# Kernel tuning notes

Hardware: AMD Instinct MI355X
Metric: run time of the kernel (lower is better)

Reference implementation:

```python
import jax, jax.numpy as jnp
import numpy as np

D = 160          # volume side
WIN = 32         # spatial window size (box filter, matches fftconvolve with ones kernel)
NUM_MIN = 100    # minimum count constraint (constraint.min_number_from_ratio)
K_CCL = 16       # fixed number of 6-neighbor min-propagation sweeps (CCL definition)
NUM_BINS = 4096  # fixed histogram bins replacing data-dependent np.unique
VALUES = (0, 1, 2)
LIST_LABELS = (1,)
NUM_LABELS = 2
HALF = WIN // 2


def _box1d(x, w, ax):
    # 'same' box-sum along one axis via cumsum (== fftconvolve with ones(w))
    left = w // 2
    right = w - 1 - left
    x = jnp.moveaxis(x, ax, -1)
    pads = [(0, 0)] * (x.ndim - 1) + [(left, right)]
    c = jnp.cumsum(jnp.pad(x, pads), axis=-1)
    c = jnp.pad(c, [(0, 0)] * (x.ndim - 1) + [(1, 0)])
    out = c[..., w:] - c[..., :-w]
    return jnp.moveaxis(out, -1, ax)


def box_sum(x, w):
    for ax in range(x.ndim):
        x = _box1d(x, w, ax)
    return x


def _shift(a, s, ax, fill):
    # shift by s along ax, filling vacated border with `fill`
    r = jnp.roll(a, s, axis=ax)
    n = a.shape[ax]
    co = jnp.arange(n).reshape([n if i == ax else 1 for i in range(a.ndim)])
    bad = (co < s) if s > 0 else (co >= n + s)
    return jnp.where(bad, fill, r)


def label_size_map(seg):
    # create_label_size_map: connected-component labeling (6-connectivity,
    # K_CCL min-propagation sweeps) then replace each component by its size.
    n_vox = seg.size
    big = jnp.int32(n_vox + 2)
    idx = (jnp.arange(n_vox, dtype=jnp.int32) + 1).reshape(seg.shape)
    lab0 = jnp.where(seg, idx, big)

    def step(_, lab):
        m = lab
        for ax in range(seg.ndim):
            for s in (1, -1):
                m = jnp.minimum(m, _shift(lab, s, ax, big))
        return jnp.where(seg, m, big)

    lab = jax.lax.fori_loop(0, K_CCL, step, lab0)
    labels = jnp.where(seg, lab, 0)  # background -> label 0
    cnt = jnp.zeros(n_vox + 1, jnp.float32).at[labels.ravel()].add(1.0)
    return jnp.where(seg, cnt[labels], 0.0)


def _proba_weights(candidates, mean_list):
    # create_probability_weights: reciprocal-histogram weighting over rounded
    # mean component sizes (fixed NUM_BINS integer bins; bin 0 = non-candidate).
    pw = jnp.ones_like(candidates)
    for m in mean_list:
        possible = candidates * m
        idx = jnp.clip(jnp.round(possible), 0, NUM_BINS - 1).astype(jnp.int32)
        hist = jnp.zeros(NUM_BINS, jnp.float32).at[idx.ravel()].add(1.0)
        numb = jnp.sum(hist[1:])
        rec = jnp.where(hist[1:] > 0, numb / jnp.maximum(hist[1:], 1.0), 0.0)
        ph = rec / jnp.sum(rec)
        ph_full = jnp.concatenate([jnp.zeros(1, jnp.float32), ph])
        pw = pw * ph_full[idx]
    return pw / jnp.sum(pw)


def setup_inputs() -> dict:
    key = jax.random.key(0)
    data = jax.random.randint(key, (D, D, D), 0, 3).astype(jnp.float32)
    return {"data": data}


def reference(data):
    data = jnp.round(data)
    inner = tuple(s - 2 * HALF for s in data.shape)
    final = jnp.pad(jnp.ones(inner, jnp.float32), [(HALF, HALF)] * 3)
    mean_list = []
    valid_others = []
    for v in VALUES:
        seg = data == v
        segf = seg.astype(jnp.float32)
        lsize = label_size_map(seg)
        cw = box_sum(segf, WIN)                              # counts_window
        valid = (cw > max(NUM_MIN, 1)).astype(jnp.float32)   # valid_places
        cs = box_sum(lsize * valid, WIN)                     # counts_size
        mean = jnp.where(cw > 0, cs / jnp.maximum(cw, 1.0), 0.0)
        if v in LIST_LABELS:
            mean_list.append(mean)
            final = final * valid
        else:
            valid_others.append(valid)
    for vo in valid_others:
        final = final + vo
    num_labels_add = max(NUM_LABELS - len(LIST_LABELS), 0)
    candidates = (final >= num_labels_add + 1).astype(jnp.float32)
    proba_fin = _proba_weights(candidates, mean_list)
    return candidates, proba_fin
```

## Files before the change

kernel.cpp:

```cpp
#include <hip/hip_runtime.h>
#include <cmath>

#define D 160
#define DD (D*D)
#define NVOX (D*D*D)
#define BIGV (NVOX + 2)
#define NBINS 4096
#define HALF 16
#define RGRID 800
#define SGRID 1000
#define ZGRID 1000
#define CGRID 800

template<int MODE>
__device__ __forceinline__ void rot_block(
    const void* __restrict__ vin, unsigned* __restrict__ out, int bi, int tid)
{
    __shared__ unsigned tin[32][161];
    __shared__ unsigned filt[160][33];
    int L0 = bi * 32;
    size_t base = (size_t)L0 * D;

    if (MODE == 0) {
        const float4* s4 = (const float4*)((const float*)vin + base);
        for (int i = tid; i < 32 * (D / 4); i += 512) {
            float4 v = s4[i];
            int e = i * 4, r = e / D, c = e - r * D;
            float rr;
            rr = rintf(v.x); tin[r][c]   = (rr==0.f) | ((rr==1.f)?0x10000u:0u);
            rr = rintf(v.y); tin[r][c+1] = (rr==0.f) | ((rr==1.f)?0x10000u:0u);
            rr = rintf(v.z); tin[r][c+2] = (rr==0.f) | ((rr==1.f)?0x10000u:0u);
            rr = rintf(v.w); tin[r][c+3] = (rr==0.f) | ((rr==1.f)?0x10000u:0u);
        }
    } else {
        const uint4* s4 = (const uint4*)((const unsigned*)vin + base);
        for (int i = tid; i < 32 * (D / 4); i += 512) {
            uint4 v = s4[i];
            int e = i * 4, r = e / D, c = e - r * D;
            tin[r][c] = v.x; tin[r][c+1] = v.y; tin[r][c+2] = v.z; tin[r][c+3] = v.w;
        }
    }
    __syncthreads();

    {
        int r = tid & 31, s = tid >> 5;
        int i0 = 10 * s;
        const unsigned* ln = tin[r];
        unsigned sum = 0u;
        int jlo = i0 - 16; if (jlo < 0) jlo = 0;
        int jhi = i0 + 15; if (jhi > D - 1) jhi = D - 1;
        for (int j = jlo; j <= jhi; ++j) sum += ln[j];
        #pragma unroll
        for (int k = 0; k < 10; ++k) {
            int i = i0 + k;
            filt[i][r] = sum;
            int add = i + 16, rem = i - 16;
            if (add <= D - 1) sum += ln[add];
            if (rem >= 0)     sum -= ln[rem];
        }
    }
    __syncthreads();

    int r = tid & 31;
    for (int c = (tid >> 5); c < D; c += 16)
        out[(size_t)c * DD + L0 + r] = filt[c][r];
}

__global__ __launch_bounds__(256) void box_rot_f32_g_kernel(
    const int* __restrict__ lab, const int* __restrict__ cnt,
    const unsigned* __restrict__ cwp, float* __restrict__ out)
{
    __shared__ float tin[32][161];
    __shared__ float filt[160][33];
    int L0 = blockIdx.x * 32;
    size_t base = (size_t)L0 * D;

    const int4*  lab4 = (const int4*)(lab + base);
    const uint4* cw4  = (const uint4*)(cwp + base);
    for (int i = threadIdx.x; i < 32 * (D / 4); i += 256) {
        int4 l = lab4[i];
        uint4 cw = cw4[i];
        int e = i * 4, r = e / D, c = e - r * D;
        tin[r][c]   = (l.x != BIGV && (cw.x >> 16) > 100u) ? (float)cnt[l.x] : 0.f;
        tin[r][c+1] = (l.y != BIGV && (cw.y >> 16) > 100u) ? (float)cnt[l.y] : 0.f;
        tin[r][c+2] = (l.z != BIGV && (cw.z >> 16) > 100u) ? (float)cnt[l.z] : 0.f;
        tin[r][c+3] = (l.w != BIGV && (cw.w >> 16) > 100u) ? (float)cnt[l.w] : 0.f;
    }
    __syncthreads();

    {
        int r = threadIdx.x & 31, s = threadIdx.x >> 5;
        int i0 = 20 * s;
        const float* ln = tin[r];
        float sum = 0.f;
        int jlo = i0 - 16; if (jlo < 0) jlo = 0;
        int jhi = i0 + 15; if (jhi > D - 1) jhi = D - 1;
        for (int j = jlo; j <= jhi; ++j) sum += ln[j];
        #pragma unroll 4
        for (int k = 0; k < 20; ++k) {
            int i = i0 + k;
            filt[i][r] = sum;
            int add = i + 16, rem = i - 16;
            if (add <= D - 1) sum += ln[add];
            if (rem >= 0)     sum -= ln[rem];
        }
    }
    __syncthreads();

    int r = threadIdx.x & 31;
    for (int c = (threadIdx.x >> 5); c < D; c += 8)
        out[(size_t)c * DD + L0 + r] = filt[c][r];
}

__global__ __launch_bounds__(256) void box_rot_f32_kernel(
    const float* __restrict__ fin, float* __restrict__ out)
{
    __shared__ float tin[32][161];
    __shared__ float filt[160][33];
    int L0 = blockIdx.x * 32;
    size_t base = (size_t)L0 * D;

    const float4* s4 = (const float4*)(fin + base);
    for (int i = threadIdx.x; i < 32 * (D / 4); i += 256) {
        float4 v = s4[i];
        int e = i * 4, r = e / D, c = e - r * D;
        tin[r][c] = v.x; tin[r][c+1] = v.y; tin[r][c+2] = v.z; tin[r][c+3] = v.w;
    }
    __syncthreads();

    {
        int r = threadIdx.x & 31, s = threadIdx.x >> 5;
        int i0 = 20 * s;
        const float* ln = tin[r];
        float sum = 0.f;
        int jlo = i0 - 16; if (jlo < 0) jlo = 0;
        int jhi = i0 + 15; if (jhi > D - 1) jhi = D - 1;
        for (int j = jlo; j <= jhi; ++j) sum += ln[j];
        #pragma unroll 4
        for (int k = 0; k < 20; ++k) {
            int i = i0 + k;
            filt[i][r] = sum;
            int add = i + 16, rem = i - 16;
            if (add <= D - 1) sum += ln[add];
            if (rem >= 0)     sum -= ln[rem];
        }
    }
    __syncthreads();

    int r = threadIdx.x & 31;
    for (int c = (threadIdx.x >> 5); c < D; c += 8)
        out[(size_t)c * DD + L0 + r] = filt[c][r];
}

__global__ __launch_bounds__(256) void box_rot_fin_kernel(
    const float* __restrict__ fin, const unsigned* __restrict__ cwp,
    unsigned short* __restrict__ idxbuf, int* __restrict__ partial)
{
    __shared__ float tin[32][161];
    __shared__ float filt[160][33];
    __shared__ int lh[NBINS];
    for (int i = threadIdx.x; i < NBINS; i += 256) lh[i] = 0;

    int L0 = blockIdx.x * 32;
    size_t base = (size_t)L0 * D;
    const float4* s4 = (const float4*)(fin + base);
    for (int i = threadIdx.x; i < 32 * (D / 4); i += 256) {
        float4 v = s4[i];
        int e = i * 4, r = e / D, c = e - r * D;
        tin[r][c] = v.x; tin[r][c+1] = v.y; tin[r][c+2] = v.z; tin[r][c+3] = v.w;
    }
    __syncthreads();

    {
        int r = threadIdx.x & 31, s = threadIdx.x >> 5;
        int i0 = 20 * s;
        const float* ln = tin[r];
        float sum = 0.f;
        int jlo = i0 - 16; if (jlo < 0) jlo = 0;
        int jhi = i0 + 15; if (jhi > D - 1) jhi = D - 1;
        for (int j = jlo; j <= jhi; ++j) sum += ln[j];
        #pragma unroll 4
        for (int k = 0; k < 20; ++k) {
            int i = i0 + k;
            filt[i][r] = sum;
            int add = i + 16, rem = i - 16;
            if (add <= D - 1) sum += ln[add];
            if (rem >= 0)     sum -= ln[rem];
        }
    }
    __syncthreads();

    int r = threadIdx.x & 31;
    int L = L0 + r;
    int y = L / D, z = L - (L / D) * D;
    bool byz = (y >= HALF && y < D - HALF && z >= HALF && z < D - HALF);
    int wy = min(y + 15, D - 1) - max(y - 16, 0) + 1;
    int wz = min(z + 15, D - 1) - max(z - 16, 0) + 1;
    for (int c = (threadIdx.x >> 5); c < D; c += 8) {
        int p = c * DD + L;
        unsigned pk = cwp[p];
        unsigned cw0 = pk & 0xFFFFu;
        unsigned cw1 = pk >> 16;
        int wx = min(c + 15, D - 1) - max(c - 16, 0) + 1;
        unsigned cw2 = (unsigned)(wx * wy * wz) - cw0 - cw1;
        float v0 = (cw0 > 100u) ? 1.f : 0.f;
        float v1 = (cw1 > 100u) ? 1.f : 0.f;
        float v2 = (cw2 > 100u) ? 1.f : 0.f;
        float border = (byz && c >= HALF && c < D - HALF) ? 1.f : 0.f;
        float cd = (border * v1 + v0 + v2 >= 2.f) ? 1.f : 0.f;
        float mean = (cw1 > 0u) ? filt[c][r] / fmaxf((float)cw1, 1.f) : 0.f;
        int idx = (int)rintf(cd * mean);
        idx = min(max(idx, 0), NBINS - 1);
        idxbuf[p] = (unsigned short)idx;
        if (idx != 0) atomicAdd(&lh[idx], 1);
    }
    __syncthreads();
    int* po = partial + blockIdx.x * NBINS;
    for (int i = threadIdx.x; i < NBINS; i += 256) po[i] = lh[i];
}

__device__ __forceinline__ int min6(int c, int a, int b, int d, int e, int f, int g) {
    if (c == BIGV) return BIGV;
    return min(min(min(c, a), min(b, d)), min(min(e, f), g));
}

__device__ __forceinline__ int4 min7_run(int4 c, int lm, int rm,
                                         int4 ym, int4 yp, int4 xm, int4 xp) {
    int4 o;
    o.x = min6(c.x, lm,  c.y, ym.x, yp.x, xm.x, xp.x);
    o.y = min6(c.y, c.x, c.z, ym.y, yp.y, xm.y, xp.y);
    o.z = min6(c.z, c.y, c.w, ym.z, yp.z, xm.z, xp.z);
    o.w = min6(c.w, c.z, rm,  ym.w, yp.w, xm.w, xp.w);
    return o;
}

__device__ __forceinline__ void wave_count(int l, int lane, int* __restrict__ cnt) {
    unsigned long long remaining = __ballot(l != BIGV);
    while (remaining) {
        int leader = __ffsll((unsigned long long)remaining) - 1;
        int ll = __shfl(l, leader, 64);
        unsigned long long mm = __ballot(l == ll);
        if (lane == leader) atomicAdd(&cnt[ll], (int)__popcll(mm & remaining));
        remaining &= ~mm;
    }
}

__device__ __forceinline__ int4 cls4(float4 v, int p0) {
    int4 l;
    l.x = (rintf(v.x) == 1.f) ? (p0 + 1) : BIGV;
    l.y = (rintf(v.y) == 1.f) ? (p0 + 2) : BIGV;
    l.z = (rintf(v.z) == 1.f) ? (p0 + 3) : BIGV;
    l.w = (rintf(v.w) == 1.f) ? (p0 + 4) : BIGV;
    return l;
}

struct LabLd {
    const int* __restrict__ a;
    __device__ __forceinline__ int4 v(int p) const { return ((const int4*)a)[p >> 2]; }
    __device__ __forceinline__ int  s(int p) const { return a[p]; }
};
struct DataLd {
    const float* __restrict__ a;
    __device__ __forceinline__ int4 v(int p) const { return cls4(((const float4*)a)[p >> 2], p); }
    __device__ __forceinline__ int  s(int p) const { return (rintf(a[p]) == 1.f) ? (p + 1) : BIGV; }
};

template<typename LDT, int COUNT>
__device__ __forceinline__ void sweep_block(
    LDT ld, int* __restrict__ outp, int* __restrict__ cnt, int b, int tid)
{
    const int4 BIG4 = make_int4(BIGV, BIGV, BIGV, BIGV);
    int sb = (b & 7) * (SGRID / 8) + (b >> 3);
    int lane = tid & 63;
    int wv   = tid >> 6;
    int wbase = sb * 4096 + wv * 512;
    int pA = wbase + 4 * lane;
    int pB = pA + 256;

    int4 cA = ld.v(pA), cB = ld.v(pB);

    int zA = pA % D, zB = pB % D;
    int lmA = __shfl_up(cA.w, 1);
    int rmA = __shfl_down(cA.x, 1);
    int lmB = __shfl_up(cB.w, 1);
    int rmB = __shfl_down(cB.x, 1);
    int stA = __shfl(cB.x, 0, 64);
    int stB = __shfl(cA.w, 63, 64);
    if (lane == 63) rmA = stA;
    if (lane == 0)  lmB = stB;
    if (zA == 0)          lmA = BIGV;
    else if (lane == 0)   lmA = ld.s(pA - 1);
    if (zA == D - 4)      rmA = BIGV;
    if (zB == 0)          lmB = BIGV;
    if (zB == D - 4)      rmB = BIGV;
    else if (lane == 63)  rmB = ld.s(pB + 4);

    int rA = pA / D, yA = rA % D, xA = rA / D;
    int4 ylA = (yA > 0)     ? ld.v(pA - D)  : BIG4;
    int4 yhA = (yA < D - 1) ? ld.v(pA + D)  : BIG4;
    int4 xlA = (xA > 0)     ? ld.v(pA - DD) : BIG4;
    int4 xhA = (xA < D - 1) ? ld.v(pA + DD) : BIG4;
    int4 oA = min7_run(cA, lmA, rmA, ylA, yhA, xlA, xhA);

    int rB = pB / D, yB = rB % D, xB = rB / D;
    int4 ylB = (yB > 0)     ? ld.v(pB - D)  : BIG4;
    int4 yhB = (yB < D - 1) ? ld.v(pB + D)  : BIG4;
    int4 xlB = (xB > 0)     ? ld.v(pB - DD) : BIG4;
    int4 xhB = (xB < D - 1) ? ld.v(pB + DD) : BIG4;
    int4 oB = min7_run(cB, lmB, rmB, ylB, yhB, xlB, xhB);

    int4* out4 = (int4*)outp;
    out4[pA >> 2] = oA; out4[pB >> 2] = oB;

    if (COUNT) {
        wave_count(oA.x, lane, cnt);
        wave_count(oA.y, lane, cnt);
        wave_count(oA.z, lane, cnt);
        wave_count(oA.w, lane, cnt);
        wave_count(oB.x, lane, cnt);
        wave_count(oB.y, lane, cnt);
        wave_count(oB.z, lane, cnt);
        wave_count(oB.w, lane, cnt);
    }
}

__global__ __launch_bounds__(512) void ccl_sweep_kernel(
    const int* __restrict__ lab, int* __restrict__ outp)
{
    LabLd ld{lab};
    sweep_block<LabLd, 0>(ld, outp, nullptr, blockIdx.x, threadIdx.x);
}

__global__ __launch_bounds__(512) void ccl_sweep_count_kernel(
    const int* __restrict__ lab, int* __restrict__ outp, int* __restrict__ cnt)
{
    LabLd ld{lab};
    sweep_block<LabLd, 1>(ld, outp, cnt, blockIdx.x, threadIdx.x);
}

template<int MODE>
__global__ __launch_bounds__(512) void sweep_rot_kernel(
    const float* __restrict__ data, const int* __restrict__ labsrc,
    int* __restrict__ swdst,
    const void* __restrict__ rin, unsigned* __restrict__ rout)
{
    if ((int)blockIdx.x < SGRID) {
        if (MODE == 0) {
            DataLd ld{data};
            sweep_block<DataLd, 0>(ld, swdst, nullptr, blockIdx.x, threadIdx.x);
        } else {
            LabLd ld{labsrc};
            sweep_block<LabLd, 0>(ld, swdst, nullptr, blockIdx.x, threadIdx.x);
        }
    } else {
        rot_block<MODE>(rin, rout, blockIdx.x - SGRID, threadIdx.x);
    }
}

__global__ __launch_bounds__(512) void sweep_zero_kernel(
    const int* __restrict__ labsrc, int* __restrict__ swdst,
    int* __restrict__ zbuf, int* __restrict__ ticket)
{
    if ((int)blockIdx.x < SGRID) {
        LabLd ld{labsrc};
        sweep_block<LabLd, 0>(ld, swdst, nullptr, blockIdx.x, threadIdx.x);
    } else {
        int zb = blockIdx.x - SGRID;
        int t = (zb * 512 + threadIdx.x) * 2;
        const int4 z4 = make_int4(0, 0, 0, 0);
        ((int4*)zbuf)[t] = z4; ((int4*)zbuf)[t + 1] = z4;
        if (zb == 0 && threadIdx.x == 0) { zbuf[NVOX] = 0; ticket[0] = 0; }
    }
}

__global__ __launch_bounds__(512) void sweep_cand_kernel(
    const int* __restrict__ labsrc, int* __restrict__ swdst,
    const unsigned* __restrict__ cwp, float* __restrict__ cand)
{
    if ((int)blockIdx.x < SGRID) {
        LabLd ld{labsrc};
        sweep_block<LabLd, 0>(ld, swdst, nullptr, blockIdx.x, threadIdx.x);
        return;
    }
    int t0 = (blockIdx.x - SGRID) * 512 + threadIdx.x;
    const uint4* cw4 = (const uint4*)cwp;
    float4* c4 = (float4*)cand;
    for (int q = t0; q < NVOX / 4; q += CGRID * 512) {
        int p0 = q * 4;
        int z0 = p0 % D;
        int r  = p0 / D;
        int y  = r % D;
        int x  = r / D;
        int wy = min(y + 15, D - 1) - max(y - 16, 0) + 1;
        int wx = min(x + 15, D - 1) - max(x - 16, 0) + 1;
        bool bxy = (y >= HALF && y < D - HALF && x >= HALF && x < D - HALF);
        uint4 pk = cw4[q];
        float4 o;
        {
            unsigned c0 = pk.x & 0xFFFFu, c1 = pk.x >> 16;
            int z = z0, wz = min(z + 15, D - 1) - max(z - 16, 0) + 1;
            unsigned c2 = (unsigned)(wx * wy * wz) - c0 - c1;
            float v0 = (c0 > 100u) ? 1.f : 0.f, v1 = (c1 > 100u) ? 1.f : 0.f, v2 = (c2 > 100u) ? 1.f : 0.f;
            float border = (bxy && z >= HALF && z < D - HALF) ? 1.f : 0.f;
            o.x = (border * v1 + v0 + v2 >= 2.f) ? 1.f : 0.f;
        }
        {
            unsigned c0 = pk.y & 0xFFFFu, c1 = pk.y >> 16;
            int z = z0 + 1, wz = min(z + 15, D - 1) - max(z - 16, 0) + 1;
            unsigned c2 = (unsigned)(wx * wy * wz) - c0 - c1;
            float v0 = (c0 > 100u) ? 1.f : 0.f, v1 = (c1 > 100u) ? 1.f : 0.f, v2 = (c2 > 100u) ? 1.f : 0.f;
            float border = (bxy && z >= HALF && z < D - HALF) ? 1.f : 0.f;
            o.y = (border * v1 + v0 + v2 >= 2.f) ? 1.f : 0.f;
        }
        {
            unsigned c0 = pk.z & 0xFFFFu, c1 = pk.z >> 16;
            int z = z0 + 2, wz = min(z + 15, D - 1) - max(z - 16, 0) + 1;
            unsigned c2 = (unsigned)(wx * wy * wz) - c0 - c1;
            float v0 = (c0 > 100u) ? 1.f : 0.f, v1 = (c1 > 100u) ? 1.f : 0.f, v2 = (c2 > 100u) ? 1.f : 0.f;
            float border = (bxy && z >= HALF && z < D - HALF) ? 1.f : 0.f;
            o.z = (border * v1 + v0 + v2 >= 2.f) ? 1.f : 0.f;
        }
        {
            unsigned c0 = pk.w & 0xFFFFu, c1 = pk.w >> 16;
            int z = z0 + 3, wz = min(z + 15, D - 1) - max(z - 16, 0) + 1;
            unsigned c2 = (unsigned)(wx * wy * wz) - c0 - c1;
            float v0 = (c0 > 100u) ? 1.f : 0.f, v1 = (c1 > 100u) ? 1.f : 0.f, v2 = (c2 > 100u) ? 1.f : 0.f;
            float border = (bxy && z >= HALF && z < D - HALF) ? 1.f : 0.f;
            o.w = (border * v1 + v0 + v2 >= 2.f) ? 1.f : 0.f;
        }
        c4[q] = o;
    }
}

__global__ __launch_bounds__(256) void hist_rp_kernel(
    const int* __restrict__ partial, int* __restrict__ hist,
    float* __restrict__ ph_full, float* __restrict__ Sout,
    int* __restrict__ ticket)
{
    int t = threadIdx.x;
    int bin = blockIdx.x * 256 + t;
    int s = 0;
    #pragma unroll 4
    for (int b = 0; b < RGRID; ++b) s += partial[b * NBINS + bin];
    __hip_atomic_store(&hist[bin], s, __ATOMIC_RELAXED, __HIP_MEMORY_SCOPE_AGENT);
    __threadfence();
    __syncthreads();
    __shared__ int lastblk;
    if (t == 0) lastblk = (atomicAdd(ticket, 1) == gridDim.x - 1) ? 1 : 0;
    __syncthreads();
    if (!lastblk) return;

    __shared__ float red[256];
    int hv[16];
    #pragma unroll
    for (int k = 0; k < 16; ++k)
        hv[k] = __hip_atomic_load(&hist[t + k * 256], __ATOMIC_RELAXED,
                                  __HIP_MEMORY_SCOPE_AGENT);

    float loc = 0.f;
    #pragma unroll
    for (int k = 0; k < 16; ++k) {
        int b = t + k * 256;
        if (b >= 1) loc += (float)hv[k];
    }
    red[t] = loc; __syncthreads();
    for (int o = 128; o > 0; o >>= 1) { if (t < o) red[t] += red[t + o]; __syncthreads(); }
    float numb = red[0]; __syncthreads();

    float rv[16];
    loc = 0.f;
    #pragma unroll
    for (int k = 0; k < 16; ++k) {
        int b = t + k * 256;
        float r = 0.f;
        if (b >= 1) {
            int h = hv[k];
            if (h > 0) r = numb / (float)h;
        }
        rv[k] = r;
        loc += r;
    }
    red[t] = loc; __syncthreads();
    for (int o = 128; o > 0; o >>= 1) { if (t < o) red[t] += red[t + o]; __syncthreads(); }
    float sumrec = red[0]; __syncthreads();
    float inv_sumrec = (sumrec > 0.f) ? 1.f / sumrec : 0.f;

    loc = 0.f;
    #pragma unroll
    for (int k = 0; k < 16; ++k) {
        int b = t + k * 256;
        float ph = (b >= 1) ? rv[k] * inv_sumrec : 0.f;
        ph_full[b] = ph;
        loc += ph * (float)hv[k];
    }
    red[t] = loc; __syncthreads();
    for (int o = 128; o > 0; o >>= 1) { if (t < o) red[t] += red[t + o]; __syncthreads(); }
    if (t == 0) Sout[0] = (red[0] > 0.f) ? red[0] : 1.f;
}

__global__ __launch_bounds__(256) void proba_kernel(
    const unsigned short* __restrict__ idxbuf,
    const float* __restrict__ ph_full, const float* __restrict__ Sv,
    float* __restrict__ outp)
{
    int t = blockIdx.x * blockDim.x + threadIdx.x;
    ushort4 i4 = ((const ushort4*)idxbuf)[t];
    float inv = 1.f / Sv[0];
    float4 o;
    o.x = ph_full[i4.x] * inv;
    o.y = ph_full[i4.y] * inv;
    o.z = ph_full[i4.z] * inv;
    o.w = ph_full[i4.w] * inv;
    ((float4*)outp)[t] = o;
}

extern "C" void kernel_launch(void* const* d_in, const int* in_sizes, int n_in,
                              void* d_out, int out_size, void* d_ws, size_t ws_size,
                              hipStream_t stream)
{
    const float* data = (const float*)d_in[0];
    float* out   = (float*)d_out;
    float* cand  = out;
    float* proba = out + NVOX;

    char* ws = (char*)d_ws;
    const size_t NB = (size_t)NVOX * sizeof(float);
    float* W1 = (float*)(ws);
    float* W2 = (float*)(ws + NB);
    float* W3 = (float*)(ws + 2 * NB);
    int*   W4 = (int*)(ws + 3 * NB);
    int*   cnt  = W4;
    float* ph   = (float*)(ws + 4 * NB + 16);
    int*   hist = (int*)  (ws + 4 * NB + 16 + NBINS * 4);
    float* Sv   = (float*)(ws + 4 * NB + 16 + 2 * NBINS * 4);
    int*   ticket = (int*)(ws + 4 * NB + 16 + 2 * NBINS * 4 + 8);
    unsigned short* idxbuf = (unsigned short*)cnt;
    int* partial = (int*)W2;

    dim3 rb(256), rg(RGRID);
    dim3 sbk(512);
    dim3 sg(SGRID);
    dim3 srg(SGRID + RGRID);
    dim3 szg(SGRID + ZGRID);
    dim3 scg(SGRID + CGRID);
    dim3 pb(256), pg(NVOX / 4 / 256);

    sweep_rot_kernel<0><<<srg, sbk, 0, stream>>>(data, nullptr, (int*)W2,
                                                 data, (unsigned*)W1);
    sweep_rot_kernel<1><<<srg, sbk, 0, stream>>>(nullptr, (int*)W2, W4,
                                                 W1, (unsigned*)W3);
    sweep_rot_kernel<1><<<srg, sbk, 0, stream>>>(nullptr, W4, (int*)W2,
                                                 W3, (unsigned*)W1);
    unsigned* cwp = (unsigned*)W1;

    sweep_zero_kernel<<<szg, sbk, 0, stream>>>((int*)W2, (int*)W3, W4, ticket);

    sweep_cand_kernel<<<scg, sbk, 0, stream>>>((int*)W3, (int*)W2, cwp, cand);

    for (int i = 0; i < 10; ++i) {
        const int* src = (i & 1) ? (int*)W3 : (int*)W2;
        int*       dst = (i & 1) ? (int*)W2 : (int*)W3;
        ccl_sweep_kernel<<<sg, sbk, 0, stream>>>(src, dst);
    }
    ccl_sweep_count_kernel<<<sg, sbk, 0, stream>>>((int*)W2, (int*)W3, cnt);
    int* lab = (int*)W3;

    box_rot_f32_g_kernel<<<rg, rb, 0, stream>>>(lab, cnt, cwp, W2);
    box_rot_f32_kernel<<<rg, rb, 0, stream>>>(W2, W3);
    box_rot_fin_kernel<<<rg, rb, 0, stream>>>(W3, cwp, idxbuf, partial);

    hist_rp_kernel<<<dim3(16), dim3(256), 0, stream>>>(partial, hist, ph, Sv, ticket);
    proba_kernel<<<pg, pb, 0, stream>>>(idxbuf, ph, Sv, proba);
}
```

Baseline: 386.8 us.

## Fuse z and y box-sum passes into one per-plane kernel using 2D prefix sums

Replaces the three rotating box-filter kernels with two. The first kernel loads a whole x-plane into shared memory, prefix-sums along z and slides a window along y. The second applies the x-window directly in the finalize/histogram kernel, which removes one full-volume write/read pass and one launch. The plane kernel runs only 160 blocks with 160 active threads each, and its serial prefix loop gives little parallelism. That may lower occupancy compared with the previous 800-block grid.

```diff
diff --git a/kernel.cpp b/kernel.cpp
--- a/kernel.cpp
+++ b/kernel.cpp
@@ -8,6 +8,7 @@
 #define NBINS 4096
 #define HALF 16
 #define RGRID 800
+#define FGRID 800
 #define SGRID 1000
 #define ZGRID 1000
 #define CGRID 800
@@ -66,153 +67,109 @@
         out[(size_t)c * DD + L0 + r] = filt[c][r];
 }
 
-__global__ __launch_bounds__(256) void box_rot_f32_g_kernel(
+__global__ __launch_bounds__(256) void plane_zy_g_kernel(
     const int* __restrict__ lab, const int* __restrict__ cnt,
     const unsigned* __restrict__ cwp, float* __restrict__ out)
 {
-    __shared__ float tin[32][161];
-    __shared__ float filt[160][33];
-    int L0 = blockIdx.x * 32;
-    size_t base = (size_t)L0 * D;
-
+    __shared__ float tin[160][161];
+    int x = blockIdx.x;
+    size_t base = (size_t)x * DD;
     const int4*  lab4 = (const int4*)(lab + base);
     const uint4* cw4  = (const uint4*)(cwp + base);
-    for (int i = threadIdx.x; i < 32 * (D / 4); i += 256) {
+    for (int i = threadIdx.x; i < DD / 4; i += 256) {
         int4 l = lab4[i];
         uint4 cw = cw4[i];
-        int e = i * 4, r = e / D, c = e - r * D;
-        tin[r][c]   = (l.x != BIGV && (cw.x >> 16) > 100u) ? (float)cnt[l.x] : 0.f;
-        tin[r][c+1] = (l.y != BIGV && (cw.y >> 16) > 100u) ? (float)cnt[l.y] : 0.f;
-        tin[r][c+2] = (l.z != BIGV && (cw.z >> 16) > 100u) ? (float)cnt[l.z] : 0.f;
-        tin[r][c+3] = (l.w != BIGV && (cw.w >> 16) > 100u) ? (float)cnt[l.w] : 0.f;
-    }
-    __syncthreads();
-
-    {
-        int r = threadIdx.x & 31, s = threadIdx.x >> 5;
-        int i0 = 20 * s;
-        const float* ln = tin[r];
-        float sum = 0.f;
-        int jlo = i0 - 16; if (jlo < 0) jlo = 0;
-        int jhi = i0 + 15; if (jhi > D - 1) jhi = D - 1;
-        for (int j = jlo; j <= jhi; ++j) sum += ln[j];
-        #pragma unroll 4
-        for (int k = 0; k < 20; ++k) {
-            int i = i0 + k;
-            filt[i][r] = sum;
-            int add = i + 16, rem = i - 16;
-            if (add <= D - 1) sum += ln[add];
-            if (rem >= 0)     sum -= ln[rem];
-        }
-    }
-    __syncthreads();
-
-    int r = threadIdx.x & 31;
-    for (int c = (threadIdx.x >> 5); c < D; c += 8)
-        out[(size_t)c * DD + L0 + r] = filt[c][r];
-}
-
-__global__ __launch_bounds__(256) void box_rot_f32_kernel(
-    const float* __restrict__ fin, float* __restrict__ out)
-{
-    __shared__ float tin[32][161];
-    __shared__ float filt[160][33];
-    int L0 = blockIdx.x * 32;
-    size_t base = (size_t)L0 * D;
-
-    const float4* s4 = (const float4*)(fin + base);
-    for (int i = threadIdx.x; i < 32 * (D / 4); i += 256) {
-        float4 v = s4[i];
-        int e = i * 4, r = e / D, c = e - r * D;
-        tin[r][c] = v.x; tin[r][c+1] = v.y; tin[r][c+2] = v.z; tin[r][c+3] = v.w;
-    }
-    __syncthreads();
-
-    {
-        int r = threadIdx.x & 31, s = threadIdx.x >> 5;
-        int i0 = 20 * s;
-        const float* ln = tin[r];
-        float sum = 0.f;
-        int jlo = i0 - 16; if (jlo < 0) jlo = 0;
-        int jhi = i0 + 15; if (jhi > D - 1) jhi = D - 1;
-        for (int j = jlo; j <= jhi; ++j) sum += ln[j];
-        #pragma unroll 4
-        for (int k = 0; k < 20; ++k) {
-            int i = i0 + k;
-            filt[i][r] = sum;
-            int add = i + 16, rem = i - 16;
-            if (add <= D - 1) sum += ln[add];
-            if (rem >= 0)     sum -= ln[rem];
-        }
-    }
-    __syncthreads();
-
-    int r = threadIdx.x & 31;
-    for (int c = (threadIdx.x >> 5); c < D; c += 8)
-        out[(size_t)c * DD + L0 + r] = filt[c][r];
-}
-
-__global__ __launch_bounds__(256) void box_rot_fin_kernel(
-    const float* __restrict__ fin, const unsigned* __restrict__ cwp,
+        int e = i * 4, y = e / D, z = e - y * D;
+        tin[y][z]   = (l.x != BIGV && (cw.x >> 16) > 100u) ? (float)cnt[l.x] : 0.f;
+        tin[y][z+1] = (l.y != BIGV && (cw.y >> 16) > 100u) ? (float)cnt[l.y] : 0.f;
+        tin[y][z+2] = (l.z != BIGV && (cw.z >> 16) > 100u) ? (float)cnt[l.z] : 0.f;
+        tin[y][z+3] = (l.w != BIGV && (cw.w >> 16) > 100u) ? (float)cnt[l.w] : 0.f;
+    }
+    __syncthreads();
+
+    if (threadIdx.x < D) {
+        float p = 0.f;
+        float* row = tin[threadIdx.x];
+        for (int z = 0; z < D; ++z) { p += row[z]; row[z] = p; }
+    }
+    __syncthreads();
+
+    if (threadIdx.x < D) {
+        int c = threadIdx.x;
+        int zhi = min(c + 15, D - 1);
+        bool hl = (c >= 16);
+        int zlo = c - 16;
+        float* op = out + base + c;
+        float S = 0.f;
+        for (int u = 0; u <= 15; ++u)
+            S += tin[u][zhi] - (hl ? tin[u][zlo] : 0.f);
+        for (int y = 0; y < D; ++y) {
+            op[(size_t)y * D] = S;
+            int add = y + 16, rem = y - 16;
+            if (add <= D - 1) S += tin[add][zhi] - (hl ? tin[add][zlo] : 0.f);
+            if (rem >= 0)     S -= tin[rem][zhi] - (hl ? tin[rem][zlo] : 0.f);
+        }
+    }
+}
+
+__global__ __launch_bounds__(256) void box_fin_x_kernel(
+    const float* __restrict__ zy, const unsigned* __restrict__ cwp,
     unsigned short* __restrict__ idxbuf, int* __restrict__ partial)
 {
-    __shared__ float tin[32][161];
-    __shared__ float filt[160][33];
+    __shared__ float tile[160][33];
     __shared__ int lh[NBINS];
     for (int i = threadIdx.x; i < NBINS; i += 256) lh[i] = 0;
 
-    int L0 = blockIdx.x * 32;
-    size_t base = (size_t)L0 * D;
-    const float4* s4 = (const float4*)(fin + base);
-    for (int i = threadIdx.x; i < 32 * (D / 4); i += 256) {
-        float4 v = s4[i];
-        int e = i * 4, r = e / D, c = e - r * D;
-        tin[r][c] = v.x; tin[r][c+1] = v.y; tin[r][c+2] = v.z; tin[r][c+3] = v.w;
-    }
-    __syncthreads();
-
-    {
-        int r = threadIdx.x & 31, s = threadIdx.x >> 5;
-        int i0 = 20 * s;
-        const float* ln = tin[r];
-        float sum = 0.f;
-        int jlo = i0 - 16; if (jlo < 0) jlo = 0;
-        int jhi = i0 + 15; if (jhi > D - 1) jhi = D - 1;
-        for (int j = jlo; j <= jhi; ++j) sum += ln[j];
-        #pragma unroll 4
-        for (int k = 0; k < 20; ++k) {
-            int i = i0 + k;
-            filt[i][r] = sum;
-            int add = i + 16, rem = i - 16;
-            if (add <= D - 1) sum += ln[add];
-            if (rem >= 0)     sum -= ln[rem];
-        }
+    int b = blockIdx.x;
+    int y  = b % D;
+    int zt = b / D;
+    int z0 = zt * 32;
+    int yb = y * D + z0;
+
+    for (int i = threadIdx.x; i < D * 8; i += 256) {
+        int x = i >> 3, q = i & 7;
+        float4 v = *(const float4*)(zy + (size_t)x * DD + yb + q * 4);
+        int c = q * 4;
+        tile[x][c] = v.x; tile[x][c+1] = v.y; tile[x][c+2] = v.z; tile[x][c+3] = v.w;
     }
     __syncthreads();
 
     int r = threadIdx.x & 31;
-    int L = L0 + r;
-    int y = L / D, z = L - (L / D) * D;
+    int s = threadIdx.x >> 5;
+    int z = z0 + r;
+    int i0 = 20 * s;
     bool byz = (y >= HALF && y < D - HALF && z >= HALF && z < D - HALF);
     int wy = min(y + 15, D - 1) - max(y - 16, 0) + 1;
     int wz = min(z + 15, D - 1) - max(z - 16, 0) + 1;
-    for (int c = (threadIdx.x >> 5); c < D; c += 8) {
-        int p = c * DD + L;
+
+    float S = 0.f;
+    int jlo = i0 - 16; if (jlo < 0) jlo = 0;
+    int jhi = i0 + 15; if (jhi > D - 1) jhi = D - 1;
+    for (int j = jlo; j <= jhi; ++j) S += tile[j][r];
+
+    #pragma unroll 4
+    for (int k = 0; k < 20; ++k) {
+        int i = i0 + k;
+        int p = i * DD + y * D + z;
         unsigned pk = cwp[p];
         unsigned cw0 = pk & 0xFFFFu;
         unsigned cw1 = pk >> 16;
-        int wx = min(c + 15, D - 1) - max(c - 16, 0) + 1;
+        int wx = min(i + 15, D - 1) - max(i - 16, 0) + 1;
         unsigned cw2 = (unsigned)(wx * wy * wz) - cw0 - cw1;
         float v0 = (cw0 > 100u) ? 1.f : 0.f;
         float v1 = (cw1 > 100u) ? 1.f : 0.f;
         float v2 = (cw2 > 100u) ? 1.f : 0.f;
-        float border = (byz && c >= HALF && c < D - HALF) ? 1.f : 0.f;
+        float border = (byz && i >= HALF && i < D - HALF) ? 1.f : 0.f;
         float cd = (border * v1 + v0 + v2 >= 2.f) ? 1.f : 0.f;
-        float mean = (cw1 > 0u) ? filt[c][r] / fmaxf((float)cw1, 1.f) : 0.f;
+        float mean = (cw1 > 0u) ? S / fmaxf((float)cw1, 1.f) : 0.f;
         int idx = (int)rintf(cd * mean);
         idx = min(max(idx, 0), NBINS - 1);
         idxbuf[p] = (unsigned short)idx;
         if (idx != 0) atomicAdd(&lh[idx], 1);
+
+        int add = i + 16, rem = i - 16;
+        if (add <= D - 1) S += tile[add][r];
+        if (rem >= 0)     S -= tile[rem][r];
     }
     __syncthreads();
     int* po = partial + blockIdx.x * NBINS;
@@ -359,7 +316,7 @@
 
 __global__ __launch_bounds__(512) void sweep_zero_kernel(
     const int* __restrict__ labsrc, int* __restrict__ swdst,
-    int* __restrict__ zbuf, int* __restrict__ ticket)
+    int* __restrict__ zbuf, int* __restrict__ tickets)
 {
     if ((int)blockIdx.x < SGRID) {
         LabLd ld{labsrc};
@@ -369,7 +326,9 @@
         int t = (zb * 512 + threadIdx.x) * 2;
         const int4 z4 = make_int4(0, 0, 0, 0);
         ((int4*)zbuf)[t] = z4; ((int4*)zbuf)[t + 1] = z4;
-        if (zb == 0 && threadIdx.x == 0) { zbuf[NVOX] = 0; ticket[0] = 0; }
+        if (zb == 0 && threadIdx.x == 0) {
+            zbuf[NVOX] = 0; tickets[0] = 0; tickets[1] = 0;
+        }
     }
 }
 
@@ -441,7 +400,7 @@
     int bin = blockIdx.x * 256 + t;
     int s = 0;
     #pragma unroll 4
-    for (int b = 0; b < RGRID; ++b) s += partial[b * NBINS + bin];
+    for (int b = 0; b < FGRID; ++b) s += partial[b * NBINS + bin];
     __hip_atomic_store(&hist[bin], s, __ATOMIC_RELAXED, __HIP_MEMORY_SCOPE_AGENT);
     __threadfence();
     __syncthreads();
@@ -533,11 +492,10 @@
     float* ph   = (float*)(ws + 4 * NB + 16);
     int*   hist = (int*)  (ws + 4 * NB + 16 + NBINS * 4);
     float* Sv   = (float*)(ws + 4 * NB + 16 + 2 * NBINS * 4);
-    int*   ticket = (int*)(ws + 4 * NB + 16 + 2 * NBINS * 4 + 8);
+    int*   tickets = (int*)(ws + 4 * NB + 16 + 2 * NBINS * 4 + 8);
     unsigned short* idxbuf = (unsigned short*)cnt;
-    int* partial = (int*)W2;
-
-    dim3 rb(256), rg(RGRID);
+    int* partial = (int*)W3;
+
     dim3 sbk(512);
     dim3 sg(SGRID);
     dim3 srg(SGRID + RGRID);
@@ -553,7 +511,7 @@
                                                  W3, (unsigned*)W1);
     unsigned* cwp = (unsigned*)W1;
 
-    sweep_zero_kernel<<<szg, sbk, 0, stream>>>((int*)W2, (int*)W3, W4, ticket);
+    sweep_zero_kernel<<<szg, sbk, 0, stream>>>((int*)W2, (int*)W3, W4, tickets);
 
     sweep_cand_kernel<<<scg, sbk, 0, stream>>>((int*)W3, (int*)W2, cwp, cand);
 
@@ -565,10 +523,10 @@
     ccl_sweep_count_kernel<<<sg, sbk, 0, stream>>>((int*)W2, (int*)W3, cnt);
     int* lab = (int*)W3;
 
-    box_rot_f32_g_kernel<<<rg, rb, 0, stream>>>(lab, cnt, cwp, W2);
-    box_rot_f32_kernel<<<rg, rb, 0, stream>>>(W2, W3);
-    box_rot_fin_kernel<<<rg, rb, 0, stream>>>(W3, cwp, idxbuf, partial);
-
-    hist_rp_kernel<<<dim3(16), dim3(256), 0, stream>>>(partial, hist, ph, Sv, ticket);
+    plane_zy_g_kernel<<<dim3(D), dim3(256), 0, stream>>>(lab, cnt, cwp, W2);
+    box_fin_x_kernel<<<dim3(FGRID), dim3(256), 0, stream>>>(W2, cwp, idxbuf, partial);
+
+    hist_rp_kernel<<<dim3(16), dim3(256), 0, stream>>>(partial, hist, ph, Sv,
+                                                       &tickets[0]);
     proba_kernel<<<pg, pb, 0, stream>>>(idxbuf, ph, Sv, proba);
 }
```

New measurement: 394.0 us. Within noise of the previous version (+1.9%).
